# Optimization experiments

Hardware: AMD Instinct MI355X
Metric: run time of the kernel (lower is better)

Reference implementation:

```python
import jax, jax.numpy as jnp
import numpy as np

N_NODES = 100000
N_EDGES = 3200000
NFEAT = 256
NHID = 256


def setup_inputs() -> dict:
    key = jax.random.key(0)
    k_x, k_ws, k_wn, k_src, k_dst = jax.random.split(key, 5)
    x = jax.random.normal(k_x, (N_NODES, NFEAT), dtype=jnp.float32)
    W_self = jax.random.normal(k_ws, (NFEAT, NHID), dtype=jnp.float32) * (1.0 / np.sqrt(NFEAT))
    W_neigh = jax.random.normal(k_wn, (NFEAT, NHID), dtype=jnp.float32) * (1.0 / np.sqrt(NFEAT))
    b = jnp.zeros((NHID,), dtype=jnp.float32)
    edge_src = jax.random.randint(k_src, (N_EDGES,), 0, N_NODES, dtype=jnp.int32)
    edge_dst = jax.random.randint(k_dst, (N_EDGES,), 0, N_NODES, dtype=jnp.int32)
    return {"x": x, "W_self": W_self, "W_neigh": W_neigh, "b": b,
            "edge_src": edge_src, "edge_dst": edge_dst}


def reference(x, W_self, W_neigh, b, edge_src, edge_dst):
    n = x.shape[0]
    # mean aggregation over incoming edges: gather src feats, scatter-add to dst
    msg = x[edge_src]                                              # [E, F]
    agg = jax.ops.segment_sum(msg, edge_dst, num_segments=n)       # [N, F]
    deg = jax.ops.segment_sum(jnp.ones_like(edge_dst, dtype=x.dtype),
                              edge_dst, num_segments=n)            # [N]
    h_neigh = agg / jnp.maximum(deg, 1.0)[:, None]                 # mean (0 for isolated)
    # SAGEConv 'mean': fc_self(x) + fc_neigh(h_neigh) (bias on neigh branch)
    out = x @ W_self + h_neigh @ W_neigh + b                       # [N, H]
    return jax.nn.relu(out)
```

## Files before the change

kernel.cpp:

```cpp
#include <hip/hip_runtime.h>
#include <stdint.h>

typedef __attribute__((ext_vector_type(8))) short bf16x8;
typedef __attribute__((ext_vector_type(4))) float f32x4;
typedef __attribute__((ext_vector_type(2))) float f32x2;

#define NF 256
#define NH 256
#define KTOT 512
#define BM 128
#define BK 64
#define EB 512
#define NBIN 512

static __device__ __forceinline__ unsigned short f2bf(float f){
  union { float f; unsigned int u; } v; v.f = f;
  unsigned int r = v.u + 0x7fffu + ((v.u >> 16) & 1u);
  return (unsigned short)(r >> 16);
}
static __device__ __forceinline__ unsigned int f2e4(float f){
  union { float f; unsigned int u; } v; v.f = f;
  unsigned int s = v.u >> 31;
  unsigned int mag = v.u & 0x7fffffffu;
  if (mag > 0x43E00000u) mag = 0x43E00000u;
  unsigned int r = mag + 0x7ffffu + ((mag >> 20) & 1u);
  if (r < 0x3C800000u) return 0u;
  return (s << 7) | (((r >> 20) - 960u) & 0x7fu);
}
static __device__ __forceinline__ ushort4 dec8(unsigned int v){
#if __has_builtin(__builtin_amdgcn_cvt_pk_f32_fp8)
  f32x2 lo = __builtin_amdgcn_cvt_pk_f32_fp8((int)v, false);
  f32x2 hi = __builtin_amdgcn_cvt_pk_f32_fp8((int)v, true);
  ushort4 o; o.x=f2bf(lo[0]); o.y=f2bf(lo[1]); o.z=f2bf(hi[0]); o.w=f2bf(hi[1]);
  return o;
#else
  ushort4 o; unsigned short r[4];
  #pragma unroll
  for (int j = 0; j < 4; j++){
    unsigned int b = (v >> (8*j)) & 0xffu;
    unsigned int tt = b & 0x7fu;
    union { unsigned int u; float f; } w;
    w.u = ((tt + 960u) << 20) | ((b & 0x80u) << 24);
    r[j] = tt ? f2bf(w.f) : (unsigned short)0;
  }
  o.x=r[0]; o.y=r[1]; o.z=r[2]; o.w=r[3];
  return o;
#endif
}
static __device__ __forceinline__ void accw(unsigned int v, f32x2& a, f32x2& b){
#if __has_builtin(__builtin_amdgcn_cvt_pk_f32_fp8)
  a += __builtin_amdgcn_cvt_pk_f32_fp8((int)v, false);
  b += __builtin_amdgcn_cvt_pk_f32_fp8((int)v, true);
#else
  #pragma unroll
  for (int j = 0; j < 4; j++){
    unsigned int bb = (v >> (8*j)) & 0xffu;
    unsigned int tt = bb & 0x7fu;
    union { unsigned int u; float f; } w;
    w.u = ((tt + 960u) << 20) | ((bb & 0x80u) << 24);
    float f = tt ? w.f : 0.f;
    if (j==0) a[0] += f; else if (j==1) a[1] += f; else if (j==2) b[0] += f; else b[1] += f;
  }
#endif
}
static __device__ __forceinline__ unsigned int pkw(f32x2 a, f32x2 b){
#if __has_builtin(__builtin_amdgcn_cvt_pk_fp8_f32)
  int t = __builtin_amdgcn_cvt_pk_fp8_f32(a[0], a[1], 0, false);
  t = __builtin_amdgcn_cvt_pk_fp8_f32(b[0], b[1], t, true);
  return (unsigned int)t;
#else
  return f2e4(a[0]) | (f2e4(a[1])<<8) | (f2e4(b[0])<<16) | (f2e4(b[1])<<24);
#endif
}
static __device__ __forceinline__ void gload16(const void* g, void* lds_wave_base, int lane){
#if __has_builtin(__builtin_amdgcn_global_load_lds)
  __builtin_amdgcn_global_load_lds(
      (const __attribute__((address_space(1))) unsigned int*)g,
      (__attribute__((address_space(3))) unsigned int*)lds_wave_base, 16, 0, 0);
  (void)lane;
#else
  *(int4*)((char*)lds_wave_base + (size_t)lane*16) = *(const int4*)g;
#endif
}

__global__ void k_cvt(const float* __restrict__ x, unsigned short* __restrict__ xb,
                      unsigned int* __restrict__ xq, int n8,
                      const float* __restrict__ Ws, const float* __restrict__ Wn,
                      unsigned short* __restrict__ Wt){
  if (blockIdx.x < 2048){
    for (int i = blockIdx.x*blockDim.x + threadIdx.x; i < n8; i += 2048*blockDim.x){
      const float4* p = (const float4*)(x + (size_t)i*8);
      float4 a = p[0], b = p[1];
      ushort4 o0, o1;
      o0.x=f2bf(a.x); o0.y=f2bf(a.y); o0.z=f2bf(a.z); o0.w=f2bf(a.w);
      o1.x=f2bf(b.x); o1.y=f2bf(b.y); o1.z=f2bf(b.z); o1.w=f2bf(b.w);
      ushort4* q = (ushort4*)(xb + (size_t)i*8);
      q[0] = o0; q[1] = o1;
      unsigned int w0 = f2e4(a.x) | (f2e4(a.y)<<8) | (f2e4(a.z)<<16) | (f2e4(a.w)<<24);
      unsigned int w1 = f2e4(b.x) | (f2e4(b.y)<<8) | (f2e4(b.z)<<16) | (f2e4(b.w)<<24);
      uint2 o; o.x = w0; o.y = w1;
      ((uint2*)xq)[i] = o;
    }
  } else {
    int t = (blockIdx.x - 2048)*blockDim.x + threadIdx.x;
    if (t < NH*KTOT){
      int n = t >> 9, k = t & 511;
      float v = (k < NF) ? Ws[(size_t)k*NH + n] : Wn[(size_t)(k-NF)*NH + n];
      Wt[t] = (unsigned short)f2bf(v);
    }
  }
}

__global__ void __launch_bounds__(256) k_bhist(const int* __restrict__ dst,
                                               int* __restrict__ H, int ne){
  __shared__ int lh[NBIN];
  int blk = blockIdx.x, t = threadIdx.x;
  for (int i = t; i < NBIN; i += 256) lh[i] = 0;
  __syncthreads();
  int chunk = (ne + EB - 1) / EB;
  int e0 = blk * chunk, e1 = ne < e0 + chunk ? ne : e0 + chunk;
  for (int e = e0 + t; e < e1; e += 256)
    atomicAdd(&lh[((unsigned)dst[e]) >> 8], 1);
  __syncthreads();
  for (int i = t; i < NBIN; i += 256) H[i*EB + blk] = lh[i];
}

__global__ void k_partial(const int* __restrict__ deg, int* __restrict__ partial, int n){
  __shared__ int sm[256];
  int b = blockIdx.x, t = threadIdx.x;
  int i0 = b*1024 + t*4;
  int s = 0;
  if (i0 + 3 < n){ int4 v = *(const int4*)(deg + i0); s = v.x+v.y+v.z+v.w; }
  else { for (int j=0;j<4;j++) if (i0+j < n) s += deg[i0+j]; }
  sm[t] = s; __syncthreads();
  for (int d = 128; d > 0; d >>= 1){ if (t < d) sm[t] += sm[t+d]; __syncthreads(); }
  if (t == 0) partial[b] = sm[0];
}

__global__ void k_scanp(int* __restrict__ partial, int nb){
  __shared__ int sm[256];
  int t = threadIdx.x;
  int v = (t < nb) ? partial[t] : 0;
  sm[t] = v; __syncthreads();
  for (int d = 1; d < 256; d <<= 1){
    int u = (t >= d) ? sm[t-d] : 0; __syncthreads();
    sm[t] += u; __syncthreads();
  }
  if (t < nb) partial[t] = sm[t] - v;
}

__global__ void k_scanapply(const int* __restrict__ deg, const int* __restrict__ partial,
                            int* __restrict__ off, int n, int ne){
  __shared__ int sm[256];
  int b = blockIdx.x, t = threadIdx.x;
  int i0 = b*1024 + t*4;
  int d0=0,d1=0,d2=0,d3=0;
  if (i0 + 3 < n){ int4 v = *(const int4*)(deg + i0); d0=v.x; d1=v.y; d2=v.z; d3=v.w; }
  else { if(i0<n)d0=deg[i0]; if(i0+1<n)d1=deg[i0+1]; if(i0+2<n)d2=deg[i0+2]; if(i0+3<n)d3=deg[i0+3]; }
  int s = d0+d1+d2+d3;
  sm[t] = s; __syncthreads();
  for (int d = 1; d < 256; d <<= 1){
    int u = (t >= d) ? sm[t-d] : 0; __syncthreads();
    sm[t] += u; __syncthreads();
  }
  int run = partial[b] + sm[t] - s;
  if (i0   < n) off[i0]   = run; run += d0;
  if (i0+1 < n) off[i0+1] = run; run += d1;
  if (i0+2 < n) off[i0+2] = run; run += d2;
  if (i0+3 < n) off[i0+3] = run;
  if (b == 0 && t == 0) off[n] = ne;
}

__global__ void __launch_bounds__(256) k_bscat(const int* __restrict__ src,
                                               const int* __restrict__ dst,
                                               const int* __restrict__ base,
                                               unsigned int* __restrict__ bkt, int ne){
  __shared__ int lc[NBIN];
  __shared__ int lb[NBIN];
  int blk = blockIdx.x, t = threadIdx.x;
  for (int i = t; i < NBIN; i += 256){ lc[i] = 0; lb[i] = base[i*EB + blk]; }
  __syncthreads();
  int chunk = (ne + EB - 1) / EB;
  int e0 = blk * chunk, e1 = ne < e0 + chunk ? ne : e0 + chunk;
  for (int e = e0 + t; e < e1; e += 256){
    int d = dst[e];
    int bin = ((unsigned)d) >> 8;
    int p = lb[bin] + atomicAdd(&lc[bin], 1);
    bkt[p] = (((unsigned)src[e]) << 8) | ((unsigned)d & 255u);
  }
}

__global__ void __launch_bounds__(256) k_csr(const unsigned int* __restrict__ bkt,
                                             const int* __restrict__ base,
                                             int* __restrict__ off, int* __restrict__ col,
                                             int nn, int ne){
  __shared__ int lh[256], sc[256], se[256], lc[256];
  int b = blockIdx.x, t = threadIdx.x;
  int n0 = base[b*EB], n1 = base[(b+1)*EB];
  lh[t] = 0; lc[t] = 0;
  __syncthreads();
  for (int e = n0 + t; e < n1; e += 256)
    atomicAdd(&lh[bkt[e] & 255u], 1);
  __syncthreads();
  int v = lh[t];
  sc[t] = v; __syncthreads();
  for (int d = 1; d < 256; d <<= 1){
    int u = (t >= d) ? sc[t-d] : 0; __syncthreads();
    sc[t] += u; __syncthreads();
  }
  int excl = sc[t] - v;
  se[t] = excl;
  int node = b*256 + t;
  if (node <= nn) off[node] = n0 + excl;
  __syncthreads();
  for (int e = n0 + t; e < n1; e += 256){
    unsigned u = bkt[e];
    int low = (int)(u & 255u);
    int r = atomicAdd(&lc[low], 1);
    col[n0 + se[low] + r] = (int)(u >> 8);
  }
}

__global__ void __launch_bounds__(256) k_agg(const unsigned int* __restrict__ xw,
                                             const int* __restrict__ off,
                                             const int* __restrict__ col,
                                             unsigned int* __restrict__ hq, int n){
  int w = threadIdx.x >> 6;
  int lane = threadIdx.x & 63;
  int node = blockIdx.x*4 + w;
  if (node >= n) return;
  int e0 = off[node], e1 = off[node+1];
  int deg = e1 - e0;
  f32x2 alo = (f32x2){0.f,0.f}, ahi = (f32x2){0.f,0.f};
  for (int c0 = 0; c0 < deg; c0 += 64){
    int len = deg - c0; if (len > 64) len = 64;
    int cv = 0;
    if (lane < len) cv = col[e0 + c0 + lane];
    int i = 0;
    for (; i + 16 <= len; i += 16){
      unsigned int u[16];
      #pragma unroll
      for (int j = 0; j < 16; j++){
        int s = __builtin_amdgcn_readlane(cv, i + j);
        u[j] = xw[(size_t)s*64 + lane];
      }
      #pragma unroll
      for (int j = 0; j < 16; j++) accw(u[j], alo, ahi);
    }
    for (; i + 4 <= len; i += 4){
      unsigned int u[4];
      #pragma unroll
      for (int j = 0; j < 4; j++){
        int s = __builtin_amdgcn_readlane(cv, i + j);
        u[j] = xw[(size_t)s*64 + lane];
      }
      #pragma unroll
      for (int j = 0; j < 4; j++) accw(u[j], alo, ahi);
    }
    for (; i < len; ++i){
      int s = __builtin_amdgcn_readlane(cv, i);
      unsigned int u0 = xw[(size_t)s*64 + lane];
      accw(u0, alo, ahi);
    }
  }
  float inv = 1.f / (float)(deg > 1 ? deg : 1);
  alo *= inv; ahi *= inv;
  hq[(size_t)node*64 + lane] = pkw(alo, ahi);
}

__global__ void __launch_bounds__(512, 4) k_gemm(const unsigned short* __restrict__ xb,
                                                 const unsigned char*  __restrict__ hq,
                                                 const unsigned short* __restrict__ Wt,
                                                 const float* __restrict__ bias,
                                                 float* __restrict__ out, int M){
  __shared__ __align__(16) unsigned short As[BM*BK];
  __shared__ __align__(16) unsigned short Bs[NH*BK];
  int t = threadIdx.x;
  int m0 = blockIdx.x * BM;
  int w = t >> 6, lane = t & 63;
  int wm = w >> 2, wn = w & 3;
  int lrow = lane & 15;
  int cgrp = (lane >> 4) * 16;
  int slot  = t & 7;

  f32x4 acc[4][4];
  #pragma unroll
  for (int i=0;i<4;i++)
    #pragma unroll
    for (int j=0;j<4;j++) acc[i][j] = (f32x4){0.f,0.f,0.f,0.f};

  for (int kk = 0; kk < KTOT; kk += BK){
    __syncthreads();
    if (kk < NF){
      #pragma unroll
      for (int p = 0; p < 2; p++){
        int flat = p*512 + t;
        int row = flat >> 3;
        const char* g = (const char*)(xb + (size_t)(m0 + row)*NF + kk)
                        + ((slot ^ (row & 7)) << 4);
        gload16(g, (char*)As + (size_t)(flat & ~63)*16, lane);
      }
    } else {
      #pragma unroll
      for (int p = 0; p < 2; p++){
        int flat = p*512 + t;
        int row = flat >> 3;
        const unsigned char* g = hq + (size_t)(m0 + row)*NF + (kk - NF)
                                 + ((slot ^ (row & 7)) << 3);
        uint2 v = *(const uint2*)g;
        ushort4 lo = dec8(v.x), hi = dec8(v.y);
        char* dstb = (char*)As + (size_t)row*128 + slot*16;
        *(ushort4*)dstb = lo;
        *(ushort4*)(dstb + 8) = hi;
      }
    }
    #pragma unroll
    for (int q = 0; q < 4; q++){
      int flat = q*512 + t;
      int row = flat >> 3;
      const char* g = (const char*)(Wt + (size_t)row*KTOT + kk)
                      + ((slot ^ (row & 7)) << 4);
      gload16(g, (char*)Bs + (size_t)(flat & ~63)*16, lane);
    }
    __syncthreads();

    #pragma unroll
    for (int ks = 0; ks < 2; ks++){
      bf16x8 af[4], bfr[4];
      #pragma unroll
      for (int mi=0;mi<4;mi++){
        int row = wm*64 + mi*16 + lrow;
        int cb = (ks*64 + cgrp) ^ ((row & 7) << 4);
        af[mi] = *(const bf16x8*)((const char*)As + (size_t)row*128 + cb);
      }
      #pragma unroll
      for (int ni=0;ni<4;ni++){
        int row = wn*64 + ni*16 + lrow;
        int cb = (ks*64 + cgrp) ^ ((row & 7) << 4);
        bfr[ni] = *(const bf16x8*)((const char*)Bs + (size_t)row*128 + cb);
      }
      #pragma unroll
      for (int mi=0;mi<4;mi++)
        #pragma unroll
        for (int ni=0;ni<4;ni++)
          acc[mi][ni] = __builtin_amdgcn_mfma_f32_16x16x32_bf16(af[mi], bfr[ni], acc[mi][ni], 0, 0, 0);
    }
  }

  #pragma unroll
  for (int ni=0;ni<4;ni++){
    int cn = wn*64 + ni*16 + lrow;
    float bv = bias[cn];
    #pragma unroll
    for (int mi=0;mi<4;mi++){
      #pragma unroll
      for (int r=0;r<4;r++){
        int rm = m0 + wm*64 + mi*16 + (lane>>4)*4 + r;
        if (rm < M){
          float v = acc[mi][ni][r] + bv;
          out[(size_t)rm*NH + cn] = v > 0.f ? v : 0.f;
        }
      }
    }
  }
}

extern "C" void kernel_launch(void* const* d_in, const int* in_sizes, int n_in,
                              void* d_out, int out_size, void* d_ws, size_t ws_size,
                              hipStream_t stream){
  const float* x      = (const float*)d_in[0];
  const float* Wself  = (const float*)d_in[1];
  const float* Wneigh = (const float*)d_in[2];
  const float* bias   = (const float*)d_in[3];
  const int*   esrc   = (const int*)d_in[4];
  const int*   edst   = (const int*)d_in[5];
  const int nn = in_sizes[0] / NF;
  const int ne = in_sizes[4];
  const int mpad = ((nn + BM - 1) / BM) * BM;

  char* w = (char*)d_ws;
  auto alloc = [&](size_t bytes)->char*{
    char* p = w; w += (bytes + 511) & ~size_t(511); return p;
  };
  unsigned short* xb  = (unsigned short*)alloc((size_t)mpad*NF*2);
  unsigned char*  xq  = (unsigned char*)alloc((size_t)nn*NF);
  char* hq_bkt        = alloc((size_t)mpad*NF);
  int* col            = (int*)alloc((size_t)ne*4);
  int* base           = (int*)alloc(((size_t)NBIN*EB + 1)*4);
  int* off            = (int*)alloc((size_t)(nn+1)*4);
  unsigned short* Wt  = (unsigned short*)alloc((size_t)NH*KTOT*2);
  int* partial        = (int*)alloc(4096);
  unsigned int* bkt   = (unsigned int*)hq_bkt;
  unsigned char* hq   = (unsigned char*)hq_bkt;
  int* H              = col;

  const int nH = NBIN*EB;
  const int nb = nH / 1024;

  k_cvt<<<2048 + 512, 256, 0, stream>>>(x, xb, (unsigned int*)xq, nn*NF/8, Wself, Wneigh, Wt);
  k_bhist<<<EB, 256, 0, stream>>>(edst, H, ne);
  k_partial<<<nb, 256, 0, stream>>>(H, partial, nH);
  k_scanp<<<1, 256, 0, stream>>>(partial, nb);
  k_scanapply<<<nb, 256, 0, stream>>>(H, partial, base, nH, ne);
  k_bscat<<<EB, 256, 0, stream>>>(esrc, edst, base, bkt, ne);
  k_csr<<<NBIN, 256, 0, stream>>>(bkt, base, off, col, nn, ne);
  k_agg<<<(nn + 3)/4, 256, 0, stream>>>((const unsigned int*)xq, off, col, (unsigned int*)hq, nn);
  k_gemm<<<mpad/BM, 512, 0, stream>>>(xb, hq, Wt, bias, (float*)d_out, nn);
}
```

Baseline: 308.6 us.

## Slice fp8 feature table into 8 column slices for cache-resident aggregation

The fp8 copy of x is now written as 8 column slices of 32 bytes per node, each slice holding all nodes contiguously. The aggregation kernel assigns each block a slice via blockIdx&7, so concurrent blocks gather from a ~3.2MB slice that can stay in cache instead of the full 25.6MB table. Each wave now handles 8 nodes at once, with 8 lanes per node, in a grid-stride loop over a fixed grid of 2048 blocks. The trade-off is that each edge's col index is read by all 8 slices, and lanes idle when node degrees within a wave differ.

```diff
diff --git a/kernel.cpp b/kernel.cpp
--- a/kernel.cpp
+++ b/kernel.cpp
@@ -84,7 +84,7 @@
 }
 
 __global__ void k_cvt(const float* __restrict__ x, unsigned short* __restrict__ xb,
-                      unsigned int* __restrict__ xq, int n8,
+                      unsigned int* __restrict__ xq, int n8, int nn8,
                       const float* __restrict__ Ws, const float* __restrict__ Wn,
                       unsigned short* __restrict__ Wt){
   if (blockIdx.x < 2048){
@@ -98,8 +98,12 @@
       q[0] = o0; q[1] = o1;
       unsigned int w0 = f2e4(a.x) | (f2e4(a.y)<<8) | (f2e4(a.z)<<16) | (f2e4(a.w)<<24);
       unsigned int w1 = f2e4(b.x) | (f2e4(b.y)<<8) | (f2e4(b.z)<<16) | (f2e4(b.w)<<24);
+      int wi = i*2;
+      int node = wi >> 6;
+      int wr = wi & 63;
+      int slice = wr >> 3, ws = wr & 7;
       uint2 o; o.x = w0; o.y = w1;
-      ((uint2*)xq)[i] = o;
+      *(uint2*)(xq + (size_t)slice*nn8 + (size_t)node*8 + ws) = o;
     }
   } else {
     int t = (blockIdx.x - 2048)*blockDim.x + threadIdx.x;
@@ -221,51 +225,44 @@
   }
 }
 
-__global__ void __launch_bounds__(256) k_agg(const unsigned int* __restrict__ xw,
+__global__ void __launch_bounds__(256) k_agg(const unsigned int* __restrict__ xs,
                                              const int* __restrict__ off,
                                              const int* __restrict__ col,
-                                             unsigned int* __restrict__ hq, int n){
+                                             unsigned int* __restrict__ hq,
+                                             int nn, int nn8){
+  int slice = blockIdx.x & 7;
+  int nb    = blockIdx.x >> 3;
   int w = threadIdx.x >> 6;
   int lane = threadIdx.x & 63;
-  int node = blockIdx.x*4 + w;
-  if (node >= n) return;
-  int e0 = off[node], e1 = off[node+1];
-  int deg = e1 - e0;
-  f32x2 alo = (f32x2){0.f,0.f}, ahi = (f32x2){0.f,0.f};
-  for (int c0 = 0; c0 < deg; c0 += 64){
-    int len = deg - c0; if (len > 64) len = 64;
-    int cv = 0;
-    if (lane < len) cv = col[e0 + c0 + lane];
-    int i = 0;
-    for (; i + 16 <= len; i += 16){
-      unsigned int u[16];
-      #pragma unroll
-      for (int j = 0; j < 16; j++){
-        int s = __builtin_amdgcn_readlane(cv, i + j);
-        u[j] = xw[(size_t)s*64 + lane];
-      }
-      #pragma unroll
-      for (int j = 0; j < 16; j++) accw(u[j], alo, ahi);
-    }
-    for (; i + 4 <= len; i += 4){
-      unsigned int u[4];
-      #pragma unroll
-      for (int j = 0; j < 4; j++){
-        int s = __builtin_amdgcn_readlane(cv, i + j);
-        u[j] = xw[(size_t)s*64 + lane];
-      }
-      #pragma unroll
-      for (int j = 0; j < 4; j++) accw(u[j], alo, ahi);
-    }
-    for (; i < len; ++i){
-      int s = __builtin_amdgcn_readlane(cv, i);
-      unsigned int u0 = xw[(size_t)s*64 + lane];
-      accw(u0, alo, ahi);
-    }
-  }
-  float inv = 1.f / (float)(deg > 1 ? deg : 1);
-  alo *= inv; ahi *= inv;
-  hq[(size_t)node*64 + lane] = pkw(alo, ahi);
+  int slot = lane >> 3, f = lane & 7;
+  const unsigned int* tbl = xs + (size_t)slice*nn8;
+  for (int g0 = (nb*4 + w)*8; g0 < nn; g0 += 8192){
+    int node = g0 + slot;
+    bool nvalid = node < nn;
+    int e0 = nvalid ? off[node]   : 0;
+    int e1 = nvalid ? off[node+1] : 0;
+    int deg = e1 - e0;
+    int md = deg;
+    md = max(md, __shfl_xor(md, 8));
+    md = max(md, __shfl_xor(md, 16));
+    md = max(md, __shfl_xor(md, 32));
+    f32x2 alo = (f32x2){0.f,0.f}, ahi = (f32x2){0.f,0.f};
+    #pragma unroll 4
+    for (int r = 0; r < md; ++r){
+      int e = e0 + r;
+      if (e < e1){
+        unsigned int cb = (unsigned int)col[e];
+        unsigned int u = tbl[(size_t)cb*8u + (unsigned)f];
+        accw(u, alo, ahi);
+      }
+    }
+    if (nvalid){
+      float inv = 1.f / (float)(deg > 1 ? deg : 1);
+      alo *= inv; ahi *= inv;
+      unsigned int word = pkw(alo, ahi);
+      __builtin_nontemporal_store(word, &hq[(size_t)node*64 + slice*8 + f]);
+    }
+  }
 }
 
 __global__ void __launch_bounds__(512, 4) k_gemm(const unsigned short* __restrict__ xb,
@@ -396,14 +393,15 @@
 
   const int nH = NBIN*EB;
   const int nb = nH / 1024;
-
-  k_cvt<<<2048 + 512, 256, 0, stream>>>(x, xb, (unsigned int*)xq, nn*NF/8, Wself, Wneigh, Wt);
+  const int nn8 = nn * 8;
+
+  k_cvt<<<2048 + 512, 256, 0, stream>>>(x, xb, (unsigned int*)xq, nn*NF/8, nn8, Wself, Wneigh, Wt);
   k_bhist<<<EB, 256, 0, stream>>>(edst, H, ne);
   k_partial<<<nb, 256, 0, stream>>>(H, partial, nH);
   k_scanp<<<1, 256, 0, stream>>>(partial, nb);
   k_scanapply<<<nb, 256, 0, stream>>>(H, partial, base, nH, ne);
   k_bscat<<<EB, 256, 0, stream>>>(esrc, edst, base, bkt, ne);
   k_csr<<<NBIN, 256, 0, stream>>>(bkt, base, off, col, nn, ne);
-  k_agg<<<(nn + 3)/4, 256, 0, stream>>>((const unsigned int*)xq, off, col, (unsigned int*)hq, nn);
+  k_agg<<<2048, 256, 0, stream>>>((const unsigned int*)xq, off, col, (unsigned int*)hq, nn, nn8);
   k_gemm<<<mpad/BM, 512, 0, stream>>>(xb, hq, Wt, bias, (float*)d_out, nn);
 }
```

After: 514.1 us. 1.67x slower.
